# Kernel optimization log

Measured on AMD Instinct MI355X. Metric: run time of the kernel, lower is better.

Reference implementation:

```python
import jax, jax.numpy as jnp
import numpy as np

B, CL, QL, D2 = 64, 1024, 128, 512  # batch, c_len, q_len, hidden_size*2


def setup_inputs() -> dict:
    key = jax.random.key(0)
    ks = jax.random.split(key, 6)
    scale = 1.0 / np.sqrt(D2)
    return {
        "c": jax.random.normal(ks[0], (B, CL, D2), jnp.float32),
        "q": jax.random.normal(ks[1], (B, QL, D2), jnp.float32),
        "w_c": jax.random.normal(ks[2], (D2,), jnp.float32) * scale,
        "b_c": jnp.zeros((1,), jnp.float32),
        "w_q": jax.random.normal(ks[3], (D2,), jnp.float32) * scale,
        "b_q": jnp.zeros((1,), jnp.float32),
        "w_cq": jax.random.normal(ks[4], (D2,), jnp.float32) * scale,
        "b_cq": jnp.zeros((1,), jnp.float32),
    }


def reference(c, q, w_c, b_c, w_q, b_q, w_cq, b_cq):
    # BiDAF trilinear similarity.
    # Source loops over q_len: att_weight_cq(c * q_i); equivalent to
    # cq[b,i,j] = sum_d c[b,i,d] * q[b,j,d] * w_cq[d] + b_cq  -> single batched matmul.
    s_c = c @ w_c + b_c  # [B, CL]
    s_q = q @ w_q + b_q  # [B, QL]
    cq = jnp.einsum("bid,bjd->bij", c * w_cq, q) + b_cq  # [B, CL, QL]
    s = s_c[:, :, None] + s_q[:, None, :] + cq  # [B, CL, QL]
    a = jax.nn.softmax(s, axis=2)
    c2q = jnp.einsum("bij,bjd->bid", a, q)  # context-to-query attention
    b_att = jax.nn.softmax(jnp.max(s, axis=2), axis=1)  # [B, CL]
    q2c = jnp.einsum("bi,bid->bd", b_att, c)[:, None, :]  # [B, 1, D2], broadcast over CL
    x = jnp.concatenate([c, c2q, c * c2q, c * q2c], axis=-1)  # [B, CL, 8H]
    return x
```

## Files before the change

kernel.cpp:

```cpp
#include <hip/hip_runtime.h>

using bf16x8 = __attribute__((ext_vector_type(8))) short;
using f32x4  = __attribute__((ext_vector_type(4))) float;

#define NB 64
#define CLN 1024
#define QLN 128
#define DDN 512

typedef __attribute__((address_space(1))) const void GAS;
typedef __attribute__((address_space(3))) void LAS;

__device__ __forceinline__ unsigned f2bf(float x){
    union { float f; unsigned u; } v; v.f = x;
    unsigned r = v.u + 0x7FFFu + ((v.u >> 16) & 1u);
    return r >> 16;
}
__device__ __forceinline__ float bf2f(unsigned short u){
    union { unsigned u; float f; } v; v.u = ((unsigned)u) << 16; return v.f;
}

__global__ __launch_bounds__(256) void k0_qprep(const float* __restrict__ q,
        unsigned short* __restrict__ qT, unsigned short* __restrict__ qbf){
    __shared__ float tile[QLN][65];
    const int b  = blockIdx.x;
    const int d0 = blockIdx.y * 64;
    const int t  = threadIdx.x;
    {
        const int col = t & 63, rg = t >> 6;
        #pragma unroll 4
        for (int p = 0; p < 32; ++p){
            int j = p*4 + rg;
            float v = q[(size_t)(b*QLN + j)*DDN + d0 + col];
            tile[j][col] = v;
            qbf[(size_t)(b*QLN + j)*DDN + d0 + col] = (unsigned short)f2bf(v);
        }
    }
    __syncthreads();
    {
        const int j = t & 127, dg = t >> 7;
        #pragma unroll 4
        for (int p = 0; p < 32; ++p){
            int dd = p*2 + dg;
            qT[(size_t)(b*DDN + d0 + dd)*QLN + j] = (unsigned short)f2bf(tile[j][dd]);
        }
    }
}

__global__ __launch_bounds__(256) void k0b_sq(const float* __restrict__ q,
        const float* __restrict__ w_q, float* __restrict__ sq){
    const int b = blockIdx.x;
    const int t = threadIdx.x;
    const int wave = t >> 6, lane = t & 63;
    float wv[8];
    #pragma unroll
    for (int e=0;e<8;++e) wv[e] = w_q[lane*8+e];
    for (int j = wave; j < QLN; j += 4){
        const float* qr = q + (size_t)(b*QLN + j)*DDN + lane*8;
        float s = 0.f;
        #pragma unroll
        for (int e=0;e<8;++e) s += qr[e]*wv[e];
        #pragma unroll
        for (int m=1;m<64;m<<=1) s += __shfl_xor(s, m, 64);
        if (lane==0) sq[b*QLN + j] = s;
    }
}

__global__ __launch_bounds__(256) void k0c_cprep(const float* __restrict__ c,
        const float* __restrict__ w_c, const float* __restrict__ w_cq,
        float* out, float* __restrict__ sc_ws, float* __restrict__ inv_ws){
    const int t = threadIdx.x, lane = t & 63, w = t >> 6;
    const int row0 = blockIdx.x*32 + w*8;
    float4 wc0 = *(const float4*)(w_c  + lane*8);
    float4 wc1 = *(const float4*)(w_c  + lane*8 + 4);
    float4 wq0 = *(const float4*)(w_cq + lane*8);
    float4 wq1 = *(const float4*)(w_cq + lane*8 + 4);
    #pragma unroll 2
    for (int p=0;p<8;++p){
        const size_t gi = (size_t)(row0 + p);
        const float* cr = c + gi*DDN + lane*8;
        f32x4 a  = *(const f32x4*)cr;
        f32x4 bb = *(const f32x4*)(cr+4);
        float s = a.x*wc0.x + a.y*wc0.y + a.z*wc0.z + a.w*wc0.w
                + bb.x*wc1.x + bb.y*wc1.y + bb.z*wc1.z + bb.w*wc1.w;
        #pragma unroll
        for (int m=1;m<64;m<<=1) s += __shfl_xor(s, m, 64);
        float* orow = out + gi*2048;
        __builtin_nontemporal_store(a,  (f32x4*)(orow + lane*8));
        __builtin_nontemporal_store(bb, (f32x4*)(orow + lane*8 + 4));
        uint4 pk;
        pk.x = f2bf(a.x*wq0.x)  | (f2bf(a.y*wq0.y)  << 16);
        pk.y = f2bf(a.z*wq0.z)  | (f2bf(a.w*wq0.w)  << 16);
        pk.z = f2bf(bb.x*wq1.x) | (f2bf(bb.y*wq1.y) << 16);
        pk.w = f2bf(bb.z*wq1.z) | (f2bf(bb.w*wq1.w) << 16);
        *(uint4*)((unsigned short*)(orow + 1792) + lane*8) = pk;
        if (lane==0) sc_ws[gi] = s;
    }
    if (blockIdx.x == 0){
        for (int d=t; d<DDN; d+=256){
            float wv = w_cq[d];
            inv_ws[d] = (fabsf(wv) > 1e-35f) ? 1.0f/wv : 0.0f;
        }
    }
}

__device__ __forceinline__ void stage_tile(const float* out, size_t girow0, int kc,
        unsigned short* buf, int wm, int lane){
    const int rsub = lane >> 3, c16 = lane & 7;
    #pragma unroll
    for (int r=0;r<4;++r){
        const int chunk = wm*4 + r;
        const int row   = chunk*8 + rsub;
        const int col16 = c16 ^ (row & 7);
        const unsigned short* g =
            (const unsigned short*)(out + (girow0 + row)*2048 + 1792) + kc*64 + col16*8;
        __builtin_amdgcn_global_load_lds((GAS*)g, (LAS*)(buf + chunk*512), 16, 0, 0);
    }
}

__global__ __launch_bounds__(256,3) void k1_main(
        float* out, const unsigned short* __restrict__ qbf,
        const unsigned short* __restrict__ qT, const float* __restrict__ sq_ws,
        const float* __restrict__ sc_ws, const float* __restrict__ inv_ws,
        float* __restrict__ vts, float* __restrict__ Mts, float* __restrict__ Sts){
    __shared__ unsigned short sm_u[16384];
    __shared__ float sm_vw[4][512];
    __shared__ float sm_inv[512];
    __shared__ float sm_sq[128], sm_m[128], sm_wrow[128], sm_sc[128];
    __shared__ float sm_red[8];

    const int bid  = blockIdx.x;
    const int swzb = (bid & 7)*64 + (bid >> 3);
    const int b    = swzb >> 3;
    const int tile = swzb & 7;
    const int i0   = tile * 128;
    const int t    = threadIdx.x;
    const int lane = t & 63;
    const int wm   = t >> 6;
    const int l15  = lane & 15;
    const int l4   = lane >> 4;
    const size_t girow0 = (size_t)(b*CLN + i0);

    if (t < 128){ sm_sc[t] = sc_ws[girow0 + t]; sm_sq[t] = sq_ws[b*QLN + t]; }
    sm_inv[t] = inv_ws[t]; sm_inv[t+256] = inv_ws[t+256];

    f32x4 acc[2][8];
    #pragma unroll
    for (int mi=0;mi<2;++mi)
        #pragma unroll
        for (int nj=0;nj<8;++nj) acc[mi][nj] = f32x4{0.f,0.f,0.f,0.f};

    stage_tile(out, girow0, 0, sm_u, wm, lane);
    __syncthreads();
    const unsigned short* qbbase = qbf + (size_t)b*QLN*DDN;
    for (int kc=0; kc<8; ++kc){
        const int cur = kc & 1;
        if (kc < 7) stage_tile(out, girow0, kc+1, sm_u + (cur^1)*8192, wm, lane);
        const char* abase = (const char*)sm_u + cur*16384;
        #pragma unroll
        for (int ks=0; ks<2; ++ks){
            bf16x8 af[2], bfr[8];
            #pragma unroll
            for (int mi=0;mi<2;++mi){
                const int row = wm*32 + mi*16 + l15;
                af[mi] = *(const bf16x8*)(abase + row*128 + ((ks*64 + l4*16) ^ ((row&7)<<4)));
            }
            #pragma unroll
            for (int nj=0;nj<8;++nj)
                bfr[nj] = *(const bf16x8*)(qbbase + (size_t)(nj*16+l15)*DDN + kc*64 + ks*32 + l4*8);
            #pragma unroll
            for (int mi=0;mi<2;++mi)
                #pragma unroll
                for (int nj=0;nj<8;++nj)
                    acc[mi][nj] = __builtin_amdgcn_mfma_f32_16x16x32_bf16(bfr[nj], af[mi], acc[mi][nj], 0,0,0);
        }
        __syncthreads();
    }

    f32x4 sq4[8];
    #pragma unroll
    for (int nj=0;nj<8;++nj) sq4[nj] = *(const f32x4*)(sm_sq + nj*16 + l4*4);

    #pragma unroll
    for (int mi=0;mi<2;++mi){
        const int irow = wm*32 + mi*16 + l15;
        float rmax = -1e30f;
        #pragma unroll
        for (int nj=0;nj<8;++nj){
            #pragma unroll
            for (int r=0;r<4;++r){
                float v = acc[mi][nj][r] + sq4[nj][r];
                acc[mi][nj][r] = v;
                rmax = fmaxf(rmax, v);
            }
        }
        rmax = fmaxf(rmax, __shfl_xor(rmax, 16, 64));
        rmax = fmaxf(rmax, __shfl_xor(rmax, 32, 64));
        if (l4 == 0) sm_m[irow] = sm_sc[irow] + rmax;
        float rsum = 0.f;
        #pragma unroll
        for (int nj=0;nj<8;++nj){
            #pragma unroll
            for (int r=0;r<4;++r){
                float pv = __expf(acc[mi][nj][r] - rmax);
                acc[mi][nj][r] = pv;
                rsum += pv;
            }
        }
        rsum += __shfl_xor(rsum, 16, 64);
        rsum += __shfl_xor(rsum, 32, 64);
        const float inv = 1.f / rsum;
        #pragma unroll
        for (int nj=0;nj<8;++nj){
            uint2 u;
            u.x = f2bf(acc[mi][nj][0]*inv) | (f2bf(acc[mi][nj][1]*inv) << 16);
            u.y = f2bf(acc[mi][nj][2]*inv) | (f2bf(acc[mi][nj][3]*inv) << 16);
            *(uint2*)((char*)sm_u + irow*256 + ((nj*32 + l4*8) ^ ((irow&7)<<4))) = u;
        }
    }
    __syncthreads();

    float v0 = (t < 128) ? sm_m[t] : -1e30f;
    #pragma unroll
    for (int m=1;m<64;m<<=1) v0 = fmaxf(v0, __shfl_xor(v0, m, 64));
    if (lane==0) sm_red[wm] = v0;
    __syncthreads();
    const float mt = fmaxf(sm_red[0], sm_red[1]);
    float ev = (t < 128) ? __expf(sm_m[t] - mt) : 0.f;
    if (t < 128) sm_wrow[t] = ev;
    float es = ev;
    #pragma unroll
    for (int m=1;m<64;m<<=1) es += __shfl_xor(es, m, 64);
    if (lane==0) sm_red[4+wm] = es;
    __syncthreads();
    const float St = sm_red[4]+sm_red[5]+sm_red[6]+sm_red[7];
    float wrow_reg[2];
    wrow_reg[0] = sm_wrow[wm*32 + l15];
    wrow_reg[1] = sm_wrow[wm*32 + 16 + l15];

    const unsigned short* qtbase = qT + (size_t)b*DDN*QLN;
    for (int dc=0; dc<4; ++dc){
        f32x4 acc2[8][2];
        #pragma unroll
        for (int dt=0;dt<8;++dt){ acc2[dt][0] = f32x4{0,0,0,0}; acc2[dt][1] = f32x4{0,0,0,0}; }
        #pragma unroll
        for (int jc=0; jc<4; ++jc){
            bf16x8 b2[2];
            #pragma unroll
            for (int mi=0;mi<2;++mi){
                const int irow = wm*32 + mi*16 + l15;
                b2[mi] = *(const bf16x8*)((char*)sm_u + irow*256 + ((jc*64 + l4*16) ^ ((irow&7)<<4)));
            }
            #pragma unroll
            for (int dt=0;dt<8;++dt){
                bf16x8 a2 = *(const bf16x8*)(qtbase + (size_t)(dc*128 + dt*16 + l15)*QLN + jc*32 + l4*8);
                acc2[dt][0] = __builtin_amdgcn_mfma_f32_16x16x32_bf16(a2, b2[0], acc2[dt][0], 0,0,0);
                acc2[dt][1] = __builtin_amdgcn_mfma_f32_16x16x32_bf16(a2, b2[1], acc2[dt][1], 0,0,0);
            }
        }
        #pragma unroll
        for (int dt=0; dt<8; ++dt){
            const int d0 = dc*128 + dt*16 + l4*4;
            f32x4 iv = *(const f32x4*)(sm_inv + d0);
            f32x4 vp = f32x4{0,0,0,0};
            #pragma unroll
            for (int mi=0; mi<2; ++mi){
                const int irow = wm*32 + mi*16 + l15;
                const size_t gi = girow0 + irow;
                const unsigned short* cb = (const unsigned short*)(out + gi*2048 + 1792) + d0;
                uint2 u = *(const uint2*)cb;
                f32x4 cv;
                cv.x = bf2f((unsigned short)(u.x & 0xffff)) * iv.x;
                cv.y = bf2f((unsigned short)(u.x >> 16))    * iv.y;
                cv.z = bf2f((unsigned short)(u.y & 0xffff)) * iv.z;
                cv.w = bf2f((unsigned short)(u.y >> 16))    * iv.w;
                f32x4 v = acc2[dt][mi];
                float* orow = out + gi*2048;
                __builtin_nontemporal_store(v,  (f32x4*)(orow + 512 + d0));
                f32x4 cq; cq.x=cv.x*v.x; cq.y=cv.y*v.y; cq.z=cv.z*v.z; cq.w=cv.w*v.w;
                __builtin_nontemporal_store(cq, (f32x4*)(orow + 1024 + d0));
                const float w = wrow_reg[mi];
                vp.x += w*cv.x; vp.y += w*cv.y; vp.z += w*cv.z; vp.w += w*cv.w;
            }
            #pragma unroll
            for (int m=1;m<16;m<<=1){
                vp.x += __shfl_xor(vp.x, m, 64); vp.y += __shfl_xor(vp.y, m, 64);
                vp.z += __shfl_xor(vp.z, m, 64); vp.w += __shfl_xor(vp.w, m, 64);
            }
            if (l15 == 0) *(f32x4*)(&sm_vw[wm][d0]) = vp;
        }
    }
    __syncthreads();
    for (int d=t; d<DDN; d+=256){
        float s = sm_vw[0][d] + sm_vw[1][d] + sm_vw[2][d] + sm_vw[3][d];
        vts[(size_t)(b*8 + tile)*DDN + d] = s;
    }
    if (t == 0){ Mts[b*8 + tile] = mt; Sts[b*8 + tile] = St; }
}

__global__ __launch_bounds__(256) void k3_fused(float* out,
        const float* __restrict__ vts, const float* __restrict__ Mts,
        const float* __restrict__ Sts, const float* __restrict__ inv_ws){
    __shared__ float sq2c[512];
    const int b = blockIdx.x, rg = blockIdx.y, t = threadIdx.x;

    float Mt[8]; float M = -1e30f;
    #pragma unroll
    for (int i=0;i<8;++i){ Mt[i] = Mts[b*8+i]; M = fmaxf(M, Mt[i]); }
    float coef[8]; float denom = 0.f;
    #pragma unroll
    for (int i=0;i<8;++i){ coef[i] = __expf(Mt[i]-M); denom += coef[i]*Sts[b*8+i]; }
    const float invd = 1.f/denom;
    for (int d=t; d<DDN; d+=256){
        float s = 0.f;
        #pragma unroll
        for (int i=0;i<8;++i) s += coef[i]*vts[(size_t)(b*8+i)*DDN + d];
        sq2c[d] = s * invd * inv_ws[d];
    }
    __syncthreads();

    const int rhalf = t >> 7, d4 = (t & 127)*4;
    const f32x4 s4 = *(const f32x4*)(sq2c + d4);
    #pragma unroll 4
    for (int it=0; it<32; ++it){
        const int row = rg*64 + it*2 + rhalf;
        const size_t gi = (size_t)b*CLN + row;
        const unsigned short* cb = (const unsigned short*)(out + gi*2048 + 1792) + d4;
        uint2 u = *(const uint2*)cb;
        f32x4 o;
        o.x = bf2f((unsigned short)(u.x & 0xffff)) * s4.x;
        o.y = bf2f((unsigned short)(u.x >> 16))    * s4.y;
        o.z = bf2f((unsigned short)(u.y & 0xffff)) * s4.z;
        o.w = bf2f((unsigned short)(u.y >> 16))    * s4.w;
        __syncthreads();
        __builtin_nontemporal_store(o, (f32x4*)(out + gi*2048 + 1536 + d4));
    }
}

extern "C" void kernel_launch(void* const* d_in, const int* in_sizes, int n_in,
                              void* d_out, int out_size, void* d_ws, size_t ws_size,
                              hipStream_t stream) {
    const float* c    = (const float*)d_in[0];
    const float* q    = (const float*)d_in[1];
    const float* w_c  = (const float*)d_in[2];
    const float* w_q  = (const float*)d_in[4];
    const float* w_cq = (const float*)d_in[6];
    float* out = (float*)d_out;

    char* ws = (char*)d_ws;
    unsigned short* qT  = (unsigned short*)ws;
    unsigned short* qbf = (unsigned short*)(ws + 8388608);
    float* sq  = (float*)(ws + 16777216);
    float* sc  = (float*)(ws + 16777216 + 32768);
    float* inv = (float*)(ws + 16777216 + 32768 + 262144);
    float* Mts = (float*)(ws + 16777216 + 32768 + 262144 + 2048);
    float* Sts = (float*)(ws + 16777216 + 32768 + 262144 + 4096);
    float* vts = (float*)(ws + 16777216 + 32768 + 262144 + 6144);

    k0_qprep<<<dim3(NB, 8), 256, 0, stream>>>(q, qT, qbf);
    k0b_sq<<<NB, 256, 0, stream>>>(q, w_q, sq);
    k0c_cprep<<<2048, 256, 0, stream>>>(c, w_c, w_cq, out, sc, inv);
    k1_main<<<NB*8, 256, 0, stream>>>(out, qbf, qT, sq, sc, inv, vts, Mts, Sts);
    k3_fused<<<dim3(NB, 16), 256, 0, stream>>>(out, vts, Mts, Sts, inv);
}
```

Baseline: 288.9 us.

## Halve main-kernel row tile to 64 and split q2c combine into separate kernels

The main attention kernel now processes 64 context rows per block instead of 128. That doubles the grid to 1024 blocks, halves shared memory and accumulator registers, and raises the occupancy hint to 4 blocks per CU. Per-slab softmax statistics are reduced within one wave, which removes two block barriers. The final q2c step is split into a small combine kernel plus a flat elementwise kernel that reads the bf16 c copy with wider loads. The cost is that each block reloads the q operands for half as many rows, and there is one extra kernel launch.

```diff
diff --git a/kernel.cpp b/kernel.cpp
--- a/kernel.cpp
+++ b/kernel.cpp
@@ -104,12 +104,12 @@
     }
 }
 
-__device__ __forceinline__ void stage_tile(const float* out, size_t girow0, int kc,
+__device__ __forceinline__ void stage64(const float* out, size_t girow0, int kc,
         unsigned short* buf, int wm, int lane){
     const int rsub = lane >> 3, c16 = lane & 7;
     #pragma unroll
-    for (int r=0;r<4;++r){
-        const int chunk = wm*4 + r;
+    for (int r=0;r<2;++r){
+        const int chunk = wm*2 + r;
         const int row   = chunk*8 + rsub;
         const int col16 = c16 ^ (row & 7);
         const unsigned short* g =
@@ -118,22 +118,21 @@
     }
 }
 
-__global__ __launch_bounds__(256,3) void k1_main(
+__global__ __launch_bounds__(256,4) void k1_main(
         float* out, const unsigned short* __restrict__ qbf,
         const unsigned short* __restrict__ qT, const float* __restrict__ sq_ws,
         const float* __restrict__ sc_ws, const float* __restrict__ inv_ws,
         float* __restrict__ vts, float* __restrict__ Mts, float* __restrict__ Sts){
-    __shared__ unsigned short sm_u[16384];
+    __shared__ unsigned short sm_u[8192];
     __shared__ float sm_vw[4][512];
     __shared__ float sm_inv[512];
-    __shared__ float sm_sq[128], sm_m[128], sm_wrow[128], sm_sc[128];
-    __shared__ float sm_red[8];
+    __shared__ float sm_sq[128], sm_m[64], sm_sc[64];
 
     const int bid  = blockIdx.x;
-    const int swzb = (bid & 7)*64 + (bid >> 3);
-    const int b    = swzb >> 3;
-    const int tile = swzb & 7;
-    const int i0   = tile * 128;
+    const int swzb = (bid & 7)*128 + (bid >> 3);
+    const int b    = swzb >> 4;
+    const int slab = swzb & 15;
+    const int i0   = slab * 64;
     const int t    = threadIdx.x;
     const int lane = t & 63;
     const int wm   = t >> 6;
@@ -141,147 +140,119 @@
     const int l4   = lane >> 4;
     const size_t girow0 = (size_t)(b*CLN + i0);
 
-    if (t < 128){ sm_sc[t] = sc_ws[girow0 + t]; sm_sq[t] = sq_ws[b*QLN + t]; }
+    if (t < 64) sm_sc[t] = sc_ws[girow0 + t];
+    if (t >= 128 && t < 256) sm_sq[t-128] = sq_ws[b*QLN + (t-128)];
     sm_inv[t] = inv_ws[t]; sm_inv[t+256] = inv_ws[t+256];
 
-    f32x4 acc[2][8];
-    #pragma unroll
-    for (int mi=0;mi<2;++mi)
-        #pragma unroll
-        for (int nj=0;nj<8;++nj) acc[mi][nj] = f32x4{0.f,0.f,0.f,0.f};
-
-    stage_tile(out, girow0, 0, sm_u, wm, lane);
+    f32x4 acc[8];
+    #pragma unroll
+    for (int nj=0;nj<8;++nj) acc[nj] = f32x4{0.f,0.f,0.f,0.f};
+
+    stage64(out, girow0, 0, sm_u, wm, lane);
     __syncthreads();
     const unsigned short* qbbase = qbf + (size_t)b*QLN*DDN;
+    const int arow = wm*16 + l15;
     for (int kc=0; kc<8; ++kc){
         const int cur = kc & 1;
-        if (kc < 7) stage_tile(out, girow0, kc+1, sm_u + (cur^1)*8192, wm, lane);
-        const char* abase = (const char*)sm_u + cur*16384;
+        if (kc < 7) stage64(out, girow0, kc+1, sm_u + (cur^1)*4096, wm, lane);
+        const char* abase = (const char*)(sm_u + cur*4096);
         #pragma unroll
         for (int ks=0; ks<2; ++ks){
-            bf16x8 af[2], bfr[8];
-            #pragma unroll
-            for (int mi=0;mi<2;++mi){
-                const int row = wm*32 + mi*16 + l15;
-                af[mi] = *(const bf16x8*)(abase + row*128 + ((ks*64 + l4*16) ^ ((row&7)<<4)));
-            }
+            bf16x8 af = *(const bf16x8*)(abase + arow*128 + ((ks*64 + l4*16) ^ ((arow&7)<<4)));
+            bf16x8 bfr[8];
             #pragma unroll
             for (int nj=0;nj<8;++nj)
                 bfr[nj] = *(const bf16x8*)(qbbase + (size_t)(nj*16+l15)*DDN + kc*64 + ks*32 + l4*8);
             #pragma unroll
-            for (int mi=0;mi<2;++mi)
-                #pragma unroll
-                for (int nj=0;nj<8;++nj)
-                    acc[mi][nj] = __builtin_amdgcn_mfma_f32_16x16x32_bf16(bfr[nj], af[mi], acc[mi][nj], 0,0,0);
+            for (int nj=0;nj<8;++nj)
+                acc[nj] = __builtin_amdgcn_mfma_f32_16x16x32_bf16(bfr[nj], af, acc[nj], 0,0,0);
         }
         __syncthreads();
     }
 
+    const int irow = arow;
     f32x4 sq4[8];
     #pragma unroll
     for (int nj=0;nj<8;++nj) sq4[nj] = *(const f32x4*)(sm_sq + nj*16 + l4*4);
 
-    #pragma unroll
-    for (int mi=0;mi<2;++mi){
-        const int irow = wm*32 + mi*16 + l15;
-        float rmax = -1e30f;
-        #pragma unroll
-        for (int nj=0;nj<8;++nj){
-            #pragma unroll
-            for (int r=0;r<4;++r){
-                float v = acc[mi][nj][r] + sq4[nj][r];
-                acc[mi][nj][r] = v;
-                rmax = fmaxf(rmax, v);
-            }
-        }
-        rmax = fmaxf(rmax, __shfl_xor(rmax, 16, 64));
-        rmax = fmaxf(rmax, __shfl_xor(rmax, 32, 64));
-        if (l4 == 0) sm_m[irow] = sm_sc[irow] + rmax;
-        float rsum = 0.f;
-        #pragma unroll
-        for (int nj=0;nj<8;++nj){
-            #pragma unroll
-            for (int r=0;r<4;++r){
-                float pv = __expf(acc[mi][nj][r] - rmax);
-                acc[mi][nj][r] = pv;
-                rsum += pv;
-            }
-        }
-        rsum += __shfl_xor(rsum, 16, 64);
-        rsum += __shfl_xor(rsum, 32, 64);
-        const float inv = 1.f / rsum;
-        #pragma unroll
-        for (int nj=0;nj<8;++nj){
-            uint2 u;
-            u.x = f2bf(acc[mi][nj][0]*inv) | (f2bf(acc[mi][nj][1]*inv) << 16);
-            u.y = f2bf(acc[mi][nj][2]*inv) | (f2bf(acc[mi][nj][3]*inv) << 16);
-            *(uint2*)((char*)sm_u + irow*256 + ((nj*32 + l4*8) ^ ((irow&7)<<4))) = u;
-        }
+    float rmax = -1e30f;
+    #pragma unroll
+    for (int nj=0;nj<8;++nj){
+        #pragma unroll
+        for (int r=0;r<4;++r){
+            float v = acc[nj][r] + sq4[nj][r];
+            acc[nj][r] = v;
+            rmax = fmaxf(rmax, v);
+        }
+    }
+    rmax = fmaxf(rmax, __shfl_xor(rmax, 16, 64));
+    rmax = fmaxf(rmax, __shfl_xor(rmax, 32, 64));
+    if (l4 == 0) sm_m[irow] = sm_sc[irow] + rmax;
+    float rsum = 0.f;
+    #pragma unroll
+    for (int nj=0;nj<8;++nj){
+        #pragma unroll
+        for (int r=0;r<4;++r){
+            float pv = __expf(acc[nj][r] - rmax);
+            acc[nj][r] = pv;
+            rsum += pv;
+        }
+    }
+    rsum += __shfl_xor(rsum, 16, 64);
+    rsum += __shfl_xor(rsum, 32, 64);
+    const float pinv = 1.f / rsum;
+    #pragma unroll
+    for (int nj=0;nj<8;++nj){
+        uint2 u;
+        u.x = f2bf(acc[nj][0]*pinv) | (f2bf(acc[nj][1]*pinv) << 16);
+        u.y = f2bf(acc[nj][2]*pinv) | (f2bf(acc[nj][3]*pinv) << 16);
+        *(uint2*)((char*)sm_u + irow*256 + ((nj*32 + l4*8) ^ ((irow&7)<<4))) = u;
     }
     __syncthreads();
 
-    float v0 = (t < 128) ? sm_m[t] : -1e30f;
-    #pragma unroll
-    for (int m=1;m<64;m<<=1) v0 = fmaxf(v0, __shfl_xor(v0, m, 64));
-    if (lane==0) sm_red[wm] = v0;
-    __syncthreads();
-    const float mt = fmaxf(sm_red[0], sm_red[1]);
-    float ev = (t < 128) ? __expf(sm_m[t] - mt) : 0.f;
-    if (t < 128) sm_wrow[t] = ev;
-    float es = ev;
+    float mv = sm_m[lane];
+    #pragma unroll
+    for (int m=1;m<64;m<<=1) mv = fmaxf(mv, __shfl_xor(mv, m, 64));
+    const float mt = mv;
+    float es = __expf(sm_m[lane] - mt);
     #pragma unroll
     for (int m=1;m<64;m<<=1) es += __shfl_xor(es, m, 64);
-    if (lane==0) sm_red[4+wm] = es;
-    __syncthreads();
-    const float St = sm_red[4]+sm_red[5]+sm_red[6]+sm_red[7];
-    float wrow_reg[2];
-    wrow_reg[0] = sm_wrow[wm*32 + l15];
-    wrow_reg[1] = sm_wrow[wm*32 + 16 + l15];
+    const float wrow = __expf(sm_m[irow] - mt);
+    if (t == 0){ Mts[b*16 + slab] = mt; Sts[b*16 + slab] = es; }
 
     const unsigned short* qtbase = qT + (size_t)b*DDN*QLN;
     for (int dc=0; dc<4; ++dc){
-        f32x4 acc2[8][2];
-        #pragma unroll
-        for (int dt=0;dt<8;++dt){ acc2[dt][0] = f32x4{0,0,0,0}; acc2[dt][1] = f32x4{0,0,0,0}; }
+        f32x4 acc2[8];
+        #pragma unroll
+        for (int dt=0;dt<8;++dt) acc2[dt] = f32x4{0.f,0.f,0.f,0.f};
         #pragma unroll
         for (int jc=0; jc<4; ++jc){
-            bf16x8 b2[2];
-            #pragma unroll
-            for (int mi=0;mi<2;++mi){
-                const int irow = wm*32 + mi*16 + l15;
-                b2[mi] = *(const bf16x8*)((char*)sm_u + irow*256 + ((jc*64 + l4*16) ^ ((irow&7)<<4)));
-            }
+            bf16x8 b2 = *(const bf16x8*)((char*)sm_u + irow*256 + ((jc*64 + l4*16) ^ ((irow&7)<<4)));
             #pragma unroll
             for (int dt=0;dt<8;++dt){
                 bf16x8 a2 = *(const bf16x8*)(qtbase + (size_t)(dc*128 + dt*16 + l15)*QLN + jc*32 + l4*8);
-                acc2[dt][0] = __builtin_amdgcn_mfma_f32_16x16x32_bf16(a2, b2[0], acc2[dt][0], 0,0,0);
-                acc2[dt][1] = __builtin_amdgcn_mfma_f32_16x16x32_bf16(a2, b2[1], acc2[dt][1], 0,0,0);
+                acc2[dt] = __builtin_amdgcn_mfma_f32_16x16x32_bf16(a2, b2, acc2[dt], 0,0,0);
             }
         }
         #pragma unroll
         for (int dt=0; dt<8; ++dt){
             const int d0 = dc*128 + dt*16 + l4*4;
             f32x4 iv = *(const f32x4*)(sm_inv + d0);
-            f32x4 vp = f32x4{0,0,0,0};
-            #pragma unroll
-            for (int mi=0; mi<2; ++mi){
-                const int irow = wm*32 + mi*16 + l15;
-                const size_t gi = girow0 + irow;
-                const unsigned short* cb = (const unsigned short*)(out + gi*2048 + 1792) + d0;
-                uint2 u = *(const uint2*)cb;
-                f32x4 cv;
-                cv.x = bf2f((unsigned short)(u.x & 0xffff)) * iv.x;
-                cv.y = bf2f((unsigned short)(u.x >> 16))    * iv.y;
-                cv.z = bf2f((unsigned short)(u.y & 0xffff)) * iv.z;
-                cv.w = bf2f((unsigned short)(u.y >> 16))    * iv.w;
-                f32x4 v = acc2[dt][mi];
-                float* orow = out + gi*2048;
-                __builtin_nontemporal_store(v,  (f32x4*)(orow + 512 + d0));
-                f32x4 cq; cq.x=cv.x*v.x; cq.y=cv.y*v.y; cq.z=cv.z*v.z; cq.w=cv.w*v.w;
-                __builtin_nontemporal_store(cq, (f32x4*)(orow + 1024 + d0));
-                const float w = wrow_reg[mi];
-                vp.x += w*cv.x; vp.y += w*cv.y; vp.z += w*cv.z; vp.w += w*cv.w;
-            }
+            const size_t gi = girow0 + irow;
+            const unsigned short* cb = (const unsigned short*)(out + gi*2048 + 1792) + d0;
+            uint2 u = *(const uint2*)cb;
+            f32x4 cv;
+            cv.x = bf2f((unsigned short)(u.x & 0xffff)) * iv.x;
+            cv.y = bf2f((unsigned short)(u.x >> 16))    * iv.y;
+            cv.z = bf2f((unsigned short)(u.y & 0xffff)) * iv.z;
+            cv.w = bf2f((unsigned short)(u.y >> 16))    * iv.w;
+            f32x4 v = acc2[dt];
+            float* orow = out + gi*2048;
+            __builtin_nontemporal_store(v,  (f32x4*)(orow + 512 + d0));
+            f32x4 cq; cq.x=cv.x*v.x; cq.y=cv.y*v.y; cq.z=cv.z*v.z; cq.w=cv.w*v.w;
+            __builtin_nontemporal_store(cq, (f32x4*)(orow + 1024 + d0));
+            f32x4 vp;
+            vp.x = wrow*cv.x; vp.y = wrow*cv.y; vp.z = wrow*cv.z; vp.w = wrow*cv.w;
             #pragma unroll
             for (int m=1;m<16;m<<=1){
                 vp.x += __shfl_xor(vp.x, m, 64); vp.y += __shfl_xor(vp.y, m, 64);
@@ -293,47 +264,58 @@
     __syncthreads();
     for (int d=t; d<DDN; d+=256){
         float s = sm_vw[0][d] + sm_vw[1][d] + sm_vw[2][d] + sm_vw[3][d];
-        vts[(size_t)(b*8 + tile)*DDN + d] = s;
-    }
-    if (t == 0){ Mts[b*8 + tile] = mt; Sts[b*8 + tile] = St; }
-}
-
-__global__ __launch_bounds__(256) void k3_fused(float* out,
-        const float* __restrict__ vts, const float* __restrict__ Mts,
-        const float* __restrict__ Sts, const float* __restrict__ inv_ws){
-    __shared__ float sq2c[512];
-    const int b = blockIdx.x, rg = blockIdx.y, t = threadIdx.x;
-
-    float Mt[8]; float M = -1e30f;
-    #pragma unroll
-    for (int i=0;i<8;++i){ Mt[i] = Mts[b*8+i]; M = fmaxf(M, Mt[i]); }
-    float coef[8]; float denom = 0.f;
-    #pragma unroll
-    for (int i=0;i<8;++i){ coef[i] = __expf(Mt[i]-M); denom += coef[i]*Sts[b*8+i]; }
-    const float invd = 1.f/denom;
+        vts[(size_t)(b*16 + slab)*DDN + d] = s;
+    }
+}
+
+__global__ __launch_bounds__(256) void k2_combine(const float* __restrict__ vts,
+        const float* __restrict__ Mts, const float* __restrict__ Sts,
+        float* __restrict__ q2c){
+    const int b = blockIdx.x, t = threadIdx.x;
+    float Mt[16]; float M = -1e30f;
+    #pragma unroll
+    for (int i=0;i<16;++i){ Mt[i] = Mts[b*16+i]; M = fmaxf(M, Mt[i]); }
+    float coef[16]; float denom = 0.f;
+    #pragma unroll
+    for (int i=0;i<16;++i){ coef[i] = __expf(Mt[i]-M); denom += coef[i]*Sts[b*16+i]; }
+    const float inv = 1.f/denom;
     for (int d=t; d<DDN; d+=256){
         float s = 0.f;
         #pragma unroll
-        for (int i=0;i<8;++i) s += coef[i]*vts[(size_t)(b*8+i)*DDN + d];
-        sq2c[d] = s * invd * inv_ws[d];
-    }
-    __syncthreads();
-
-    const int rhalf = t >> 7, d4 = (t & 127)*4;
-    const f32x4 s4 = *(const f32x4*)(sq2c + d4);
-    #pragma unroll 4
-    for (int it=0; it<32; ++it){
-        const int row = rg*64 + it*2 + rhalf;
-        const size_t gi = (size_t)b*CLN + row;
-        const unsigned short* cb = (const unsigned short*)(out + gi*2048 + 1792) + d4;
-        uint2 u = *(const uint2*)cb;
-        f32x4 o;
-        o.x = bf2f((unsigned short)(u.x & 0xffff)) * s4.x;
-        o.y = bf2f((unsigned short)(u.x >> 16))    * s4.y;
-        o.z = bf2f((unsigned short)(u.y & 0xffff)) * s4.z;
-        o.w = bf2f((unsigned short)(u.y >> 16))    * s4.w;
+        for (int i=0;i<16;++i) s += coef[i]*vts[(size_t)(b*16+i)*DDN + d];
+        q2c[b*DDN + d] = s*inv;
+    }
+}
+
+__global__ __launch_bounds__(256) void k3_cq2c(float* out,
+        const float* __restrict__ q2c, const float* __restrict__ inv_ws){
+    const int t = threadIdx.x;
+    const int rloc = t >> 6, ch = t & 63;
+    for (int pass=0; pass<8; ++pass){
+        const size_t rb = (size_t)blockIdx.x + (size_t)pass*2048;
+        const size_t gi = rb*4 + rloc;
+        const int b = (int)(gi >> 10);
+        const unsigned short* cb = (const unsigned short*)(out + gi*2048 + 1792) + ch*8;
+        uint4 raw = *(const uint4*)cb;
+        const float* qp = q2c + b*DDN + ch*8;
+        float4 qa = *(const float4*)qp;
+        float4 qb = *(const float4*)(qp+4);
+        const float* ip = inv_ws + ch*8;
+        float4 ia = *(const float4*)ip;
+        float4 ib = *(const float4*)(ip+4);
+        f32x4 o0, o1;
+        o0.x = bf2f((unsigned short)(raw.x & 0xffff)) * ia.x * qa.x;
+        o0.y = bf2f((unsigned short)(raw.x >> 16))    * ia.y * qa.y;
+        o0.z = bf2f((unsigned short)(raw.y & 0xffff)) * ia.z * qa.z;
+        o0.w = bf2f((unsigned short)(raw.y >> 16))    * ia.w * qa.w;
+        o1.x = bf2f((unsigned short)(raw.z & 0xffff)) * ib.x * qb.x;
+        o1.y = bf2f((unsigned short)(raw.z >> 16))    * ib.y * qb.y;
+        o1.z = bf2f((unsigned short)(raw.w & 0xffff)) * ib.z * qb.z;
+        o1.w = bf2f((unsigned short)(raw.w >> 16))    * ib.w * qb.w;
         __syncthreads();
-        __builtin_nontemporal_store(o, (f32x4*)(out + gi*2048 + 1536 + d4));
+        f32x4* wp = (f32x4*)(out + gi*2048 + 1536) + ch*2;
+        __builtin_nontemporal_store(o0, wp);
+        __builtin_nontemporal_store(o1, wp+1);
     }
 }
 
@@ -354,12 +336,14 @@
     float* sc  = (float*)(ws + 16777216 + 32768);
     float* inv = (float*)(ws + 16777216 + 32768 + 262144);
     float* Mts = (float*)(ws + 16777216 + 32768 + 262144 + 2048);
-    float* Sts = (float*)(ws + 16777216 + 32768 + 262144 + 4096);
-    float* vts = (float*)(ws + 16777216 + 32768 + 262144 + 6144);
+    float* Sts = (float*)(ws + 16777216 + 32768 + 262144 + 6144);
+    float* vts = (float*)(ws + 16777216 + 32768 + 262144 + 10240);
+    float* q2c = (float*)(ws + 16777216 + 32768 + 262144 + 10240 + 2097152);
 
     k0_qprep<<<dim3(NB, 8), 256, 0, stream>>>(q, qT, qbf);
     k0b_sq<<<NB, 256, 0, stream>>>(q, w_q, sq);
     k0c_cprep<<<2048, 256, 0, stream>>>(c, w_c, w_cq, out, sc, inv);
-    k1_main<<<NB*8, 256, 0, stream>>>(out, qbf, qT, sq, sc, inv, vts, Mts, Sts);
-    k3_fused<<<dim3(NB, 16), 256, 0, stream>>>(out, vts, Mts, Sts, inv);
-}
+    k1_main<<<1024, 256, 0, stream>>>(out, qbf, qT, sq, sc, inv, vts, Mts, Sts);
+    k2_combine<<<NB, 256, 0, stream>>>(vts, Mts, Sts, q2c);
+    k3_cq2c<<<2048, 256, 0, stream>>>(out, q2c, inv);
+}
```

After: 299.8 us. 1.04x slower.
